# Kernel tuning notes

Hardware: AMD Instinct MI355X
Metric: run time of the kernel (lower is better)

Reference implementation:

```python
import jax, jax.numpy as jnp
import numpy as np

EPS = 1e-5
NEG_SLOPE = 0.2

def _conv1x1(x, w):
    # x: (B,C,N,K), w: (O,C) -> (B,O,N,K)
    return jnp.einsum('oc,bcnk->bonk', w, x)

def _bn(x, g, b, m, v):
    scale = g / jnp.sqrt(v + EPS)
    return x * scale[None, :, None, None] + (b - m * scale)[None, :, None, None]

def _lrelu(x):
    return jnp.where(x > 0, x, NEG_SLOPE * x)

def setup_inputs() -> dict:
    key = jax.random.key(0)
    specs = {
        'x': ((8, 6, 8192, 20), 'randn'),
        'trans_w': ((64, 6), 'randn'), 'trans_g': ((64,), 'rand'), 'trans_b': ((64,), 'randn'),
        'trans_m': ((64,), 'randn'), 'trans_v': ((64,), 'rand'),
        'pos_w1': ((64, 3), 'randn'), 'pos_g': ((64,), 'rand'), 'pos_b': ((64,), 'randn'),
        'pos_m': ((64,), 'randn'), 'pos_v': ((64,), 'rand'),
        'pos_w2': ((64, 64), 'randn'), 'pos_b2': ((64,), 'randn'),
        'gate_w1': ((16, 6), 'randn'), 'gate_g': ((16,), 'rand'), 'gate_b': ((16,), 'randn'),
        'gate_m': ((16,), 'randn'), 'gate_v': ((16,), 'rand'),
        'gate_w2': ((1, 16), 'randn'), 'gate_b2': ((1,), 'ones'),
        'attn_w1': ((16, 6), 'randn'), 'attn_g': ((16,), 'rand'), 'attn_b': ((16,), 'randn'),
        'attn_m': ((16,), 'randn'), 'attn_v': ((16,), 'rand'),
        'attn_w2': ((64, 16), 'randn'), 'attn_b2': ((64,), 'randn'),
    }
    out = {}
    for i, (name, (shape, fill)) in enumerate(specs.items()):
        k = jax.random.fold_in(key, i)
        if fill == 'randn':
            out[name] = jax.random.normal(k, shape, dtype=jnp.float32) * 0.1
        elif fill == 'rand':
            out[name] = jax.random.uniform(k, shape, dtype=jnp.float32)
        else:  # ones (gate bias init to 2.0 in original; scale ones)
            out[name] = jnp.ones(shape, dtype=jnp.float32) * 2.0
    return out

def reference(x, trans_w, trans_g, trans_b, trans_m, trans_v,
              pos_w1, pos_g, pos_b, pos_m, pos_v, pos_w2, pos_b2,
              gate_w1, gate_g, gate_b, gate_m, gate_v, gate_w2, gate_b2,
              attn_w1, attn_g, attn_b, attn_m, attn_v, attn_w2, attn_b2):
    in_channels = 3
    rel_pos = x[:, in_channels:in_channels + 3, :, :]  # (B,3,N,K)
    # pos_net: conv(3->C) + BN + LReLU + conv(C->C, bias)
    pos_h = _lrelu(_bn(_conv1x1(rel_pos, pos_w1), pos_g, pos_b, pos_m, pos_v))
    pos_enc = _conv1x1(pos_h, pos_w2) + pos_b2[None, :, None, None]
    # trans: conv(2*Cin->C) + BN + LReLU
    trans_feat = _lrelu(_bn(_conv1x1(x, trans_w), trans_g, trans_b, trans_m, trans_v)) + pos_enc
    # gate_net: conv(6->16)+BN+LReLU+conv(16->1,bias)+sigmoid (dropout=0 in eval)
    gate_h = _lrelu(_bn(_conv1x1(x, gate_w1), gate_g, gate_b, gate_m, gate_v))
    gate_map = jax.nn.sigmoid(_conv1x1(gate_h, gate_w2) + gate_b2[None, :, None, None])  # (B,1,N,K)
    clean_feat = trans_feat * gate_map
    # attn_net: conv(6->16)+BN+LReLU+conv(16->C,bias), then + pos_enc, softmax over K
    attn_h = _lrelu(_bn(_conv1x1(x, attn_w1), attn_g, attn_b, attn_m, attn_v))
    attn_logits = _conv1x1(attn_h, attn_w2) + attn_b2[None, :, None, None] + pos_enc
    attn_weights = jax.nn.softmax(attn_logits, axis=-1)
    out_attn = (trans_feat * attn_weights).sum(axis=-1)  # (B,C,N)
    out_max = clean_feat.max(axis=-1)                    # (B,C,N)
    return out_attn + out_max
```

## Files before the change

### kernel.cpp

```cpp
#include <hip/hip_runtime.h>
#include <math.h>

#define NEG 0.2f
#define EPSV 1e-5f

typedef _Float16 v8h __attribute__((ext_vector_type(8)));
typedef _Float16 v4h __attribute__((ext_vector_type(4)));
typedef _Float16 v2h __attribute__((ext_vector_type(2)));
typedef __fp16   f16x2 __attribute__((ext_vector_type(2)));
typedef float    v4f __attribute__((ext_vector_type(4)));

__device__ __forceinline__ float lrelu(float v) { return fmaxf(v, NEG * v); }
__device__ __forceinline__ v4f lrelu4(v4f v) {
    return __builtin_elementwise_max(v, v * NEG);
}
__device__ __forceinline__ v2h lreluh2(v2h v) {
    return __builtin_elementwise_max(v, v * (_Float16)NEG);
}

__device__ __forceinline__ v2h pk(float a, float b) {
    union { f16x2 i; v2h o; } u;
    u.i = __builtin_amdgcn_cvt_pkrtz(a, b);
    return u.o;
}

#define MFMA32(a, b, c) __builtin_amdgcn_mfma_f32_16x16x32_f16((a), (b), (c), 0, 0, 0)
#define MFMA16(a, b, c) __builtin_amdgcn_mfma_f32_16x16x16f16((a), (b), (c), 0, 0, 0)

__global__ __launch_bounds__(256, 3)
void gsl_mfma(const float* __restrict__ x,
              const float* __restrict__ trans_w, const float* __restrict__ trans_g,
              const float* __restrict__ trans_b, const float* __restrict__ trans_m,
              const float* __restrict__ trans_v,
              const float* __restrict__ pos_w1, const float* __restrict__ pos_g,
              const float* __restrict__ pos_b, const float* __restrict__ pos_m,
              const float* __restrict__ pos_v, const float* __restrict__ pos_w2,
              const float* __restrict__ pos_b2,
              const float* __restrict__ gate_w1, const float* __restrict__ gate_g,
              const float* __restrict__ gate_b, const float* __restrict__ gate_m,
              const float* __restrict__ gate_v, const float* __restrict__ gate_w2,
              const float* __restrict__ gate_b2,
              const float* __restrict__ attn_w1, const float* __restrict__ attn_g,
              const float* __restrict__ attn_b, const float* __restrict__ attn_m,
              const float* __restrict__ attn_v, const float* __restrict__ attn_w2,
              const float* __restrict__ attn_b2,
              float* __restrict__ out)
{
    __shared__ _Float16 WH[1920];
    __shared__ _Float16 W2L[5120];
    __shared__ float    PB2[64];
    __shared__ _Float16 PHB[4][2][1152];
    __shared__ _Float16 AHB[4][2][320];

    const int tid  = threadIdx.x;
    const int wv   = tid >> 6;
    const int lane = tid & 63;
    const int p    = lane & 15;
    const int q    = lane >> 4;

    const int b  = blockIdx.x >> 7;
    const int n0 = ((blockIdx.x & 127) << 6) | (wv << 4);
    const int n  = n0 | p;

    #pragma unroll
    for (int e = 0; e < 16; ++e) {
        int idx = tid * 16 + e;
        int t   = idx >> 9;
        int rem = idx & 511;
        int pp  = rem >> 5;
        int ii  = rem & 31;
        W2L[t * 640 + pp * 40 + ii] =
            (_Float16)pos_w2[((t >> 1) * 16 + pp) * 64 + (t & 1) * 32 + ii];
    }

    if (tid < 64) {
        const int c = tid;
        float sp = pos_g[c] * rsqrtf(pos_v[c] + EPSV);
        float bp = pos_b[c] - pos_m[c] * sp;
        _Float16* row = WH + (c >> 4) * 320 + (c & 15) * 20;
        for (int k = 0; k < 20; ++k) {
            float v = (k >= 3 && k < 6) ? pos_w1[c * 3 + (k - 3)] * sp
                                        : ((k == 6) ? bp : 0.f);
            row[k] = (_Float16)v;
        }
        PB2[c] = pos_b2[c];
    } else if (tid < 80) {
        const int j = tid - 64;
        float sa = attn_g[j] * rsqrtf(attn_v[j] + EPSV);
        float ba = attn_b[j] - attn_m[j] * sa;
        _Float16* row = WH + 1280 + j * 20;
        for (int k = 0; k < 20; ++k)
            row[k] = (_Float16)((k < 6) ? attn_w1[j * 6 + k] * sa
                                        : ((k == 6) ? ba : 0.f));
    } else if (tid < 96) {
        const int j = tid - 80;
        float sg = gate_g[j] * rsqrtf(gate_v[j] + EPSV);
        float bg = gate_b[j] - gate_m[j] * sg;
        _Float16* row = WH + 1600 + j * 20;
        for (int k = 0; k < 20; ++k)
            row[k] = (_Float16)((k < 6) ? gate_w1[j * 6 + k] * sg
                                        : ((k == 6) ? bg : 0.f));
    }

    v4h WTf[4], WA2f[4], WG2f;
    #pragma unroll
    for (int mt = 0; mt < 4; ++mt) {
        const int ch = mt * 16 + p;
        #pragma unroll
        for (int i = 0; i < 4; ++i)
            WA2f[mt][i] = (_Float16)attn_w2[ch * 16 + q * 4 + i];
        float st = trans_g[ch] * rsqrtf(trans_v[ch] + EPSV);
        float bt = trans_b[ch] - trans_m[ch] * st;
        #pragma unroll
        for (int i = 0; i < 4; ++i) {
            int k = q * 4 + i;
            float v = (k < 6) ? trans_w[ch * 6 + k] * st : ((k == 6) ? bt : 0.f);
            WTf[mt][i] = (_Float16)v;
        }
    }
    #pragma unroll
    for (int i = 0; i < 4; ++i)
        WG2f[i] = (_Float16)gate_w2[4 * q + i];
    const float gb2v = gate_b2[0];

    __syncthreads();

    const _Float16* const WP1p = WH + p * 20 + q * 4;
    const _Float16* const WA1p = WH + 1280 + p * 20 + q * 4;
    const _Float16* const WG1p = WH + 1600 + p * 20 + q * 4;
    const _Float16* const W2Lp = W2L + p * 40 + q * 8;
    const float* const    PB2p = PB2 + 4 * q;

    _Float16* const PHbase = &PHB[wv][0][0];
    _Float16* const AHbase = &AHB[wv][0][0];

    const v4f zero = {0.f, 0.f, 0.f, 0.f};
    v4f den[4], num[4], cmx[4];
    #pragma unroll
    for (int mt = 0; mt < 4; ++mt) {
        den[mt] = zero; num[mt] = zero;
        cmx[mt] = (v4f){-3.4e38f, -3.4e38f, -3.4e38f, -3.4e38f};
    }

    const float* xb = x + ((size_t)(b * 6) * 8192 + n) * 20;
    const int hi = q & 1;
    const float* const s0p = xb + (size_t)(hi ? 4 : 0) * 163840;
    const float* const s1p = xb + (size_t)(hi ? 5 : 1) * 163840;
    const float* const s2p = xb + (size_t)(hi ? 4 : 2) * 163840;
    const float* const s3p = xb + (size_t)(hi ? 5 : 3) * 163840;

    auto mk = [&](float a, float bb, float cc, float dd) -> v4h {
        v2h lo = pk(a, bb);
        v2h hh = pk(cc, dd);
        if (hi) { union { unsigned u; v2h h; } t; t.u = 0x00003C00u; hh = t.h; }
        return (v4h){lo.x, lo.y, hh.x, hh.y};
    };

    float nx0 = s0p[0], nx1 = s1p[0], nx2 = s2p[0], nx3 = s3p[0];
    v4h xv_cur = mk(nx0, nx1, nx2, nx3);
    nx0 = s0p[1]; nx1 = s1p[1]; nx2 = s2p[1]; nx3 = s3p[1];

    {
        v4f php[4];
        #pragma unroll
        for (int mt = 0; mt < 4; ++mt)
            php[mt] = MFMA16(*(const v4h*)(WP1p + mt * 320), xv_cur, zero);
        v4f ahp = MFMA16(*(const v4h*)WA1p, xv_cur, zero);
        _Float16* PHW = PHbase + p * 72 + 4 * q;
        #pragma unroll
        for (int mt = 0; mt < 4; ++mt) {
            union { v4h v; v2h h[2]; } u;
            u.h[0] = lreluh2(pk(php[mt][0], php[mt][1]));
            u.h[1] = lreluh2(pk(php[mt][2], php[mt][3]));
            *(v4h*)(PHW + mt * 16) = u.v;
        }
        union { v4h v; v2h h[2]; } ua;
        ua.h[0] = lreluh2(pk(ahp[0], ahp[1]));
        ua.h[1] = lreluh2(pk(ahp[2], ahp[3]));
        *(v4h*)(AHbase + p * 20 + 4 * q) = ua.v;
    }

    #pragma unroll 1
    for (int k = 0; k < 20; ++k) {
        asm volatile("" ::: "memory");

        const int sel = k & 1;
        _Float16* PH = PHbase + sel * 1152;
        _Float16* AH = AHbase + sel * 320;
        v8h phf0 = *(const v8h*)(PH + p * 72 + 8 * q);
        v8h phf1 = *(const v8h*)(PH + p * 72 + 32 + 8 * q);
        v4h ahf  = *(const v4h*)(AH + p * 20 + 4 * q);

        v4h xv_nxt = xv_cur;
        if (k < 19) {
            xv_nxt = mk(nx0, nx1, nx2, nx3);
            const int kn = (k < 18) ? k + 2 : 19;
            nx0 = s0p[kn]; nx1 = s1p[kn]; nx2 = s2p[kn]; nx3 = s3p[kn];

            v4f php[4];
            #pragma unroll
            for (int mt = 0; mt < 4; ++mt)
                php[mt] = MFMA16(*(const v4h*)(WP1p + mt * 320), xv_nxt, zero);
            v4f ahp = MFMA16(*(const v4h*)WA1p, xv_nxt, zero);
            _Float16* PHW = PHbase + (sel ^ 1) * 1152 + p * 72 + 4 * q;
            #pragma unroll
            for (int mt = 0; mt < 4; ++mt) {
                union { v4h v; v2h h[2]; } uu;
                uu.h[0] = lreluh2(pk(php[mt][0], php[mt][1]));
                uu.h[1] = lreluh2(pk(php[mt][2], php[mt][3]));
                *(v4h*)(PHW + mt * 16) = uu.v;
            }
            union { v4h v; v2h h[2]; } ua;
            ua.h[0] = lreluh2(pk(ahp[0], ahp[1]));
            ua.h[1] = lreluh2(pk(ahp[2], ahp[3]));
            *(v4h*)(AHbase + (sel ^ 1) * 320 + p * 20 + 4 * q) = ua.v;
        }

        v4f ghp = MFMA16(*(const v4h*)WG1p, xv_cur, zero);
        union { v4h v; v2h h[2]; } ug;
        ug.h[0] = lreluh2(pk(ghp[0], ghp[1]));
        ug.h[1] = lreluh2(pk(ghp[2], ghp[3]));
        v4f gav = MFMA16(WG2f, ug.v, zero);
        const float gate = 1.f / (1.f + __expf(-(gav[0] + gb2v)));

        #pragma unroll
        for (int mt = 0; mt < 4; ++mt) {
            v8h w2a = *(const v8h*)(W2Lp + (mt * 2 + 0) * 640);
            v8h w2b = *(const v8h*)(W2Lp + (mt * 2 + 1) * 640);
            v4f pe = MFMA32(w2a, phf0, *(const v4f*)(PB2p + mt * 16));
            pe = MFMA32(w2b, phf1, pe);
            v4f tfa = MFMA16(WTf[mt], xv_cur, zero);
            v4f tfv = lrelu4(tfa) + pe;
            pe = MFMA16(WA2f[mt], ahf, pe);
            v4f e;
            #pragma unroll
            for (int r = 0; r < 4; ++r) e[r] = __expf(pe[r]);
            den[mt] += e;
            num[mt] += tfv * e;
            cmx[mt] = __builtin_elementwise_max(cmx[mt], tfv * gate);
        }
        xv_cur = xv_nxt;
    }

    #pragma unroll
    for (int mt = 0; mt < 4; ++mt) {
        #pragma unroll
        for (int r = 0; r < 4; ++r) {
            const int ch = mt * 16 + 4 * q + r;
            out[((size_t)(b * 64 + ch)) * 8192 + n] =
                num[mt][r] / den[mt][r] + cmx[mt][r];
        }
    }
}

extern "C" void kernel_launch(void* const* d_in, const int* in_sizes, int n_in,
                              void* d_out, int out_size, void* d_ws, size_t ws_size,
                              hipStream_t stream) {
    const float* x       = (const float*)d_in[0];
    const float* trans_w = (const float*)d_in[1];
    const float* trans_g = (const float*)d_in[2];
    const float* trans_b = (const float*)d_in[3];
    const float* trans_m = (const float*)d_in[4];
    const float* trans_v = (const float*)d_in[5];
    const float* pos_w1  = (const float*)d_in[6];
    const float* pos_g   = (const float*)d_in[7];
    const float* pos_b   = (const float*)d_in[8];
    const float* pos_m   = (const float*)d_in[9];
    const float* pos_v   = (const float*)d_in[10];
    const float* pos_w2  = (const float*)d_in[11];
    const float* pos_b2  = (const float*)d_in[12];
    const float* gate_w1 = (const float*)d_in[13];
    const float* gate_g  = (const float*)d_in[14];
    const float* gate_b  = (const float*)d_in[15];
    const float* gate_m  = (const float*)d_in[16];
    const float* gate_v  = (const float*)d_in[17];
    const float* gate_w2 = (const float*)d_in[18];
    const float* gate_b2 = (const float*)d_in[19];
    const float* attn_w1 = (const float*)d_in[20];
    const float* attn_g  = (const float*)d_in[21];
    const float* attn_b  = (const float*)d_in[22];
    const float* attn_m  = (const float*)d_in[23];
    const float* attn_v  = (const float*)d_in[24];
    const float* attn_w2 = (const float*)d_in[25];
    const float* attn_b2 = (const float*)d_in[26];
    float* out = (float*)d_out;

    gsl_mfma<<<1024, 256, 0, stream>>>(
        x, trans_w, trans_g, trans_b, trans_m, trans_v,
        pos_w1, pos_g, pos_b, pos_m, pos_v, pos_w2, pos_b2,
        gate_w1, gate_g, gate_b, gate_m, gate_v, gate_w2, gate_b2,
        attn_w1, attn_g, attn_b, attn_m, attn_v, attn_w2, attn_b2,
        out);
}
```

Before: 175.6 us.

## Keep pos/attn hidden activations in registers, dropping the LDS round-trip

The first-layer MFMA outputs (pos hidden and attn hidden) are now fed straight from registers as B operands of 16x16x16 MFMAs, instead of being written to a per-wave double-buffered LDS area and read back for 16x16x32 MFMAs. The pos_w2 weight layout in LDS is permuted so its K ordering matches the register layout of the MFMA accumulator. This removes the LDS stores and loads and the software pipelining, and frees LDS so occupancy can rise to 4 blocks per CU. The cost is twice as many second-layer MFMAs (16x16x16 instead of 16x16x32) and less overlap of x loads.

```diff
diff --git a/kernel.cpp b/kernel.cpp
--- a/kernel.cpp
+++ b/kernel.cpp
@@ -24,10 +24,9 @@
     return u.o;
 }
 
-#define MFMA32(a, b, c) __builtin_amdgcn_mfma_f32_16x16x32_f16((a), (b), (c), 0, 0, 0)
 #define MFMA16(a, b, c) __builtin_amdgcn_mfma_f32_16x16x16f16((a), (b), (c), 0, 0, 0)
 
-__global__ __launch_bounds__(256, 3)
+__global__ __launch_bounds__(256, 4)
 void gsl_mfma(const float* __restrict__ x,
               const float* __restrict__ trans_w, const float* __restrict__ trans_g,
               const float* __restrict__ trans_b, const float* __restrict__ trans_m,
@@ -49,8 +48,6 @@
     __shared__ _Float16 WH[1920];
     __shared__ _Float16 W2L[5120];
     __shared__ float    PB2[64];
-    __shared__ _Float16 PHB[4][2][1152];
-    __shared__ _Float16 AHB[4][2][320];
 
     const int tid  = threadIdx.x;
     const int wv   = tid >> 6;
@@ -69,8 +66,9 @@
         int rem = idx & 511;
         int pp  = rem >> 5;
         int ii  = rem & 31;
+        int c   = (t & 1) * 32 + ((ii & 7) >> 2) * 16 + ((ii >> 3) << 2) + (ii & 3);
         W2L[t * 640 + pp * 40 + ii] =
-            (_Float16)pos_w2[((t >> 1) * 16 + pp) * 64 + (t & 1) * 32 + ii];
+            (_Float16)pos_w2[((t >> 1) * 16 + pp) * 64 + c];
     }
 
     if (tid < 64) {
@@ -131,9 +129,6 @@
     const _Float16* const W2Lp = W2L + p * 40 + q * 8;
     const float* const    PB2p = PB2 + 4 * q;
 
-    _Float16* const PHbase = &PHB[wv][0][0];
-    _Float16* const AHbase = &AHB[wv][0][0];
-
     const v4f zero = {0.f, 0.f, 0.f, 0.f};
     v4f den[4], num[4], cmx[4];
     #pragma unroll
@@ -156,67 +151,34 @@
         return (v4h){lo.x, lo.y, hh.x, hh.y};
     };
 
-    float nx0 = s0p[0], nx1 = s1p[0], nx2 = s2p[0], nx3 = s3p[0];
-    v4h xv_cur = mk(nx0, nx1, nx2, nx3);
-    nx0 = s0p[1]; nx1 = s1p[1]; nx2 = s2p[1]; nx3 = s3p[1];
-
-    {
-        v4f php[4];
-        #pragma unroll
-        for (int mt = 0; mt < 4; ++mt)
-            php[mt] = MFMA16(*(const v4h*)(WP1p + mt * 320), xv_cur, zero);
-        v4f ahp = MFMA16(*(const v4h*)WA1p, xv_cur, zero);
-        _Float16* PHW = PHbase + p * 72 + 4 * q;
+    float c0 = s0p[0], c1 = s1p[0], c2 = s2p[0], c3 = s3p[0];
+
+    #pragma unroll 1
+    for (int k = 0; k < 20; ++k) {
+        asm volatile("" ::: "memory");
+
+        v4h xv = mk(c0, c1, c2, c3);
+        if (k < 19) {
+            c0 = s0p[k + 1]; c1 = s1p[k + 1];
+            c2 = s2p[k + 1]; c3 = s3p[k + 1];
+        }
+
+        v4h phB[4];
         #pragma unroll
         for (int mt = 0; mt < 4; ++mt) {
+            v4f php = MFMA16(*(const v4h*)(WP1p + mt * 320), xv, zero);
             union { v4h v; v2h h[2]; } u;
-            u.h[0] = lreluh2(pk(php[mt][0], php[mt][1]));
-            u.h[1] = lreluh2(pk(php[mt][2], php[mt][3]));
-            *(v4h*)(PHW + mt * 16) = u.v;
-        }
+            u.h[0] = lreluh2(pk(php[0], php[1]));
+            u.h[1] = lreluh2(pk(php[2], php[3]));
+            phB[mt] = u.v;
+        }
+        v4f ahp = MFMA16(*(const v4h*)WA1p, xv, zero);
         union { v4h v; v2h h[2]; } ua;
         ua.h[0] = lreluh2(pk(ahp[0], ahp[1]));
         ua.h[1] = lreluh2(pk(ahp[2], ahp[3]));
-        *(v4h*)(AHbase + p * 20 + 4 * q) = ua.v;
-    }
-
-    #pragma unroll 1
-    for (int k = 0; k < 20; ++k) {
-        asm volatile("" ::: "memory");
-
-        const int sel = k & 1;
-        _Float16* PH = PHbase + sel * 1152;
-        _Float16* AH = AHbase + sel * 320;
-        v8h phf0 = *(const v8h*)(PH + p * 72 + 8 * q);
-        v8h phf1 = *(const v8h*)(PH + p * 72 + 32 + 8 * q);
-        v4h ahf  = *(const v4h*)(AH + p * 20 + 4 * q);
-
-        v4h xv_nxt = xv_cur;
-        if (k < 19) {
-            xv_nxt = mk(nx0, nx1, nx2, nx3);
-            const int kn = (k < 18) ? k + 2 : 19;
-            nx0 = s0p[kn]; nx1 = s1p[kn]; nx2 = s2p[kn]; nx3 = s3p[kn];
-
-            v4f php[4];
-            #pragma unroll
-            for (int mt = 0; mt < 4; ++mt)
-                php[mt] = MFMA16(*(const v4h*)(WP1p + mt * 320), xv_nxt, zero);
-            v4f ahp = MFMA16(*(const v4h*)WA1p, xv_nxt, zero);
-            _Float16* PHW = PHbase + (sel ^ 1) * 1152 + p * 72 + 4 * q;
-            #pragma unroll
-            for (int mt = 0; mt < 4; ++mt) {
-                union { v4h v; v2h h[2]; } uu;
-                uu.h[0] = lreluh2(pk(php[mt][0], php[mt][1]));
-                uu.h[1] = lreluh2(pk(php[mt][2], php[mt][3]));
-                *(v4h*)(PHW + mt * 16) = uu.v;
-            }
-            union { v4h v; v2h h[2]; } ua;
-            ua.h[0] = lreluh2(pk(ahp[0], ahp[1]));
-            ua.h[1] = lreluh2(pk(ahp[2], ahp[3]));
-            *(v4h*)(AHbase + (sel ^ 1) * 320 + p * 20 + 4 * q) = ua.v;
-        }
-
-        v4f ghp = MFMA16(*(const v4h*)WG1p, xv_cur, zero);
+        const v4h ahB = ua.v;
+
+        v4f ghp = MFMA16(*(const v4h*)WG1p, xv, zero);
         union { v4h v; v2h h[2]; } ug;
         ug.h[0] = lreluh2(pk(ghp[0], ghp[1]));
         ug.h[1] = lreluh2(pk(ghp[2], ghp[3]));
@@ -225,13 +187,16 @@
 
         #pragma unroll
         for (int mt = 0; mt < 4; ++mt) {
-            v8h w2a = *(const v8h*)(W2Lp + (mt * 2 + 0) * 640);
-            v8h w2b = *(const v8h*)(W2Lp + (mt * 2 + 1) * 640);
-            v4f pe = MFMA32(w2a, phf0, *(const v4f*)(PB2p + mt * 16));
-            pe = MFMA32(w2b, phf1, pe);
-            v4f tfa = MFMA16(WTf[mt], xv_cur, zero);
+            union { v8h v; v4h h[2]; } w2a, w2b;
+            w2a.v = *(const v8h*)(W2Lp + (mt * 2 + 0) * 640);
+            w2b.v = *(const v8h*)(W2Lp + (mt * 2 + 1) * 640);
+            v4f pe = MFMA16(w2a.h[0], phB[0], *(const v4f*)(PB2p + mt * 16));
+            pe = MFMA16(w2a.h[1], phB[1], pe);
+            pe = MFMA16(w2b.h[0], phB[2], pe);
+            pe = MFMA16(w2b.h[1], phB[3], pe);
+            v4f tfa = MFMA16(WTf[mt], xv, zero);
             v4f tfv = lrelu4(tfa) + pe;
-            pe = MFMA16(WA2f[mt], ahf, pe);
+            pe = MFMA16(WA2f[mt], ahB, pe);
             v4f e;
             #pragma unroll
             for (int r = 0; r < 4; ++r) e[r] = __expf(pe[r]);
@@ -239,7 +204,6 @@
             num[mt] += tfv * e;
             cmx[mt] = __builtin_elementwise_max(cmx[mt], tfv * gate);
         }
-        xv_cur = xv_nxt;
     }
 
     #pragma unroll
```

Measured after the change: 176.1 us. Within noise of the previous version (+0.3%).
